# Optimization experiments

Hardware: AMD Instinct MI355X
Metric: run time of the kernel (lower is better)

Reference implementation:

```python
import jax, jax.numpy as jnp
import numpy as np

B, S, D = 32, 4096, 256

def setup_inputs() -> dict:
    key = jax.random.key(0)
    k1, k2, k3 = jax.random.split(key, 3)
    inputs = jax.random.normal(k1, (B, S, D), dtype=jnp.float32)
    W = jax.random.normal(k2, (D, D), dtype=jnp.float32) * 0.05  # 'random_normal' init
    b = jnp.zeros((D,), dtype=jnp.float32)
    V = jax.random.normal(k3, (D, 1), dtype=jnp.float32) * 0.05
    return {"inputs": inputs, "W": W, "b": b, "V": V}

def reference(inputs, W, b, V):
    # score: [B,S,D] = tanh(inputs @ W + b)
    score = jnp.tanh(jnp.einsum('bsd,de->bse', inputs, W) + b)
    # logits: [B,S,1]; softmax over seq axis (axis=1)
    logits = jnp.einsum('bsd,do->bso', score, V)
    attn = jax.nn.softmax(logits, axis=1)            # [B,S,1]
    # weighted sum pooling over seq -> [B,D]
    context = jnp.sum(attn * inputs, axis=1)
    return context
```

## Files before the change

kernel.cpp:

```cpp
#include <hip/hip_runtime.h>
#include <hip/hip_bf16.h>

#define DD 256
#define SS 4096

typedef __bf16 bf16x8 __attribute__((ext_vector_type(8)));
typedef float  f32x4  __attribute__((ext_vector_type(4)));

__device__ __forceinline__ float fast_tanh(float x) {
  float e = exp2f(x * 2.885390081777927f);
  return 1.0f - 2.0f / (e + 1.0f);
}

template<int CTRL>
__device__ __forceinline__ float dpp_mov(float v) {
  return __int_as_float(__builtin_amdgcn_update_dpp(0, __float_as_int(v), CTRL, 0xF, 0xF, true));
}
__device__ __forceinline__ float row16_sum(float v) {
  v += dpp_mov<0xB1>(v);
  v += dpp_mov<0x4E>(v);
  v += dpp_mov<0x124>(v);
  v += dpp_mov<0x128>(v);
  return v;
}
__device__ __forceinline__ float row16_max(float v) {
  v = fmaxf(v, dpp_mov<0xB1>(v));
  v = fmaxf(v, dpp_mov<0x4E>(v));
  v = fmaxf(v, dpp_mov<0x124>(v));
  v = fmaxf(v, dpp_mov<0x128>(v));
  return v;
}

__global__ __launch_bounds__(256) void prep_kernel(
    const float* __restrict__ W, __bf16* __restrict__ WF)
{
  const int c = blockIdx.x * 256 + threadIdx.x;
  const int lane_c = c & 63;
  const int ks  = (c >> 6) & 7;
  const int n0  = c >> 9;
  const int col = n0 * 16 + (lane_c & 15);
  const int k0  = ks * 32 + (lane_c >> 4) * 8;
  const float* wp = W + k0 * DD + col;
  bf16x8 fr;
  #pragma unroll
  for (int i = 0; i < 8; ++i) fr[i] = (__bf16)wp[i * DD];
  *reinterpret_cast<bf16x8*>(WF + (size_t)c * 8) = fr;
}

#define PACK(dst, f0, f1) { \
  bf16x8 _fr; \
  _fr[0] = (__bf16)(f0).x; _fr[1] = (__bf16)(f0).y; \
  _fr[2] = (__bf16)(f0).z; _fr[3] = (__bf16)(f0).w; \
  _fr[4] = (__bf16)(f1).x; _fr[5] = (__bf16)(f1).y; \
  _fr[6] = (__bf16)(f1).z; _fr[7] = (__bf16)(f1).w; \
  (dst) = _fr; }

#define TILE(aX, spX, n0q) { \
  const __bf16* _bp = WtF + ((size_t)((n0q) * 8 * 64 + lane)) * 8; \
  bf16x8 _bfr[8]; \
  _Pragma("unroll") \
  for (int _ks = 0; _ks < 8; ++_ks) \
    _bfr[_ks] = *reinterpret_cast<const bf16x8*>(_bp + (size_t)_ks * 512); \
  f32x4 _acc = {0.f, 0.f, 0.f, 0.f}; \
  _Pragma("unroll") \
  for (int _ks = 0; _ks < 8; ++_ks) \
    _acc = __builtin_amdgcn_mfma_f32_16x16x32_bf16(aX[_ks], _bfr[_ks], _acc, 0, 0, 0); \
  const int _col = (n0q) * 16 + lg; \
  const float _vc = Vs[_col], _bc = Bs[_col]; \
  _Pragma("unroll") \
  for (int _r = 0; _r < 4; ++_r) \
    spX[_r] += fast_tanh(_acc[_r] + _bc) * _vc; }

__global__ __launch_bounds__(1024, 1) __attribute__((amdgpu_waves_per_eu(4)))
void fused_kernel(
    const float* __restrict__ X, const __bf16* __restrict__ WF,
    const float* __restrict__ bias, const float* __restrict__ V,
    float* __restrict__ Pout, float* __restrict__ Mout, float* __restrict__ Sout)
{
  __shared__ __bf16 WtF[8192 * 8];
  __shared__ float  Pacc[16][DD];
  __shared__ float  Vs[DD];
  __shared__ float  Bs[DD];
  __shared__ float  wred[16];
  __shared__ float  sred[16];

  const int t = threadIdx.x;
  const int wave = t >> 6, lane = t & 63;
  const int g  = lane >> 4;
  const int lg = lane & 15;
  const size_t rowBase = (size_t)blockIdx.x * 512 + (size_t)wave * 32;

  float4 raw[16];
  const float* xr0 = X + (rowBase + lg) * DD;
  #pragma unroll
  for (int ks = 0; ks < 8; ++ks) {
    const float4* p = reinterpret_cast<const float4*>(xr0 + ks * 32 + g * 8);
    raw[2 * ks]     = p[0];
    raw[2 * ks + 1] = p[1];
  }

  {
    const uint4* src = reinterpret_cast<const uint4*>(WF);
    uint4* dst = reinterpret_cast<uint4*>(WtF);
    #pragma unroll
    for (int i = 0; i < 8; ++i) dst[t + i * 1024] = src[t + i * 1024];
  }
  if (t < DD) { Vs[t] = V[t]; Bs[t] = bias[t]; }
  __syncthreads();

  bf16x8 a0[8], a1[8];
  #pragma unroll
  for (int ks = 0; ks < 8; ++ks) PACK(a0[ks], raw[2 * ks], raw[2 * ks + 1]);
  const float* xr1 = X + (rowBase + 16 + lg) * DD;
  #pragma unroll
  for (int ks = 0; ks < 4; ++ks) {
    const float4* p = reinterpret_cast<const float4*>(xr1 + ks * 32 + g * 8);
    raw[2 * ks]     = p[0];
    raw[2 * ks + 1] = p[1];
  }

  float sp0[4] = {0.f,0.f,0.f,0.f};
  float sp1[4] = {0.f,0.f,0.f,0.f};

  #pragma unroll 1
  for (int n0 = 0; n0 < 8; ++n0) TILE(a0, sp0, n0);

  #pragma unroll
  for (int ks = 0; ks < 4; ++ks) PACK(a1[ks], raw[2 * ks], raw[2 * ks + 1]);
  #pragma unroll
  for (int ks = 4; ks < 8; ++ks) {
    const float4* p = reinterpret_cast<const float4*>(xr1 + ks * 32 + g * 8);
    raw[2 * (ks - 4)]     = p[0];
    raw[2 * (ks - 4) + 1] = p[1];
  }

  #pragma unroll 1
  for (int n0 = 8; n0 < 16; ++n0) TILE(a0, sp0, n0);

  #pragma unroll
  for (int ks = 4; ks < 8; ++ks) PACK(a1[ks], raw[2 * (ks - 4)], raw[2 * (ks - 4) + 1]);

  #pragma unroll 1
  for (int n0 = 0; n0 < 16; ++n0) TILE(a1, sp1, n0);

  #pragma unroll
  for (int r = 0; r < 4; ++r) { sp0[r] = row16_sum(sp0[r]); sp1[r] = row16_sum(sp1[r]); }

  const int src = ((lg >> 2) << 4) | lg;
  float l0 = 0.f, l1 = 0.f;
  #pragma unroll
  for (int r = 0; r < 4; ++r) {
    float v0 = __shfl(sp0[r], src, 64);
    float v1 = __shfl(sp1[r], src, 64);
    if ((lg & 3) == r) { l0 = v0; l1 = v1; }
  }

  float wm = row16_max(fmaxf(l0, l1));
  if (lane == 0) wred[wave] = wm;
  __syncthreads();
  float M = -1e30f;
  #pragma unroll
  for (int w = 0; w < 16; ++w) M = fmaxf(M, wred[w]);

  const float w0 = __expf(l0 - M);
  const float w1 = __expf(l1 - M);

  float se = row16_sum(w0 + w1);
  if (lane == 0) sred[wave] = se;

  #pragma unroll
  for (int ks = 0; ks < 8; ++ks) {
    float p8[8];
    #pragma unroll
    for (int i = 0; i < 8; ++i)
      p8[i] = w0 * (float)a0[ks][i] + w1 * (float)a1[ks][i];
    #pragma unroll
    for (int i = 0; i < 8; ++i) p8[i] = row16_sum(p8[i]);
    if (lg < 2) {
      float4 v = (lg == 0) ? make_float4(p8[0], p8[1], p8[2], p8[3])
                           : make_float4(p8[4], p8[5], p8[6], p8[7]);
      *reinterpret_cast<float4*>(&Pacc[wave][ks * 32 + g * 8 + lg * 4]) = v;
    }
  }
  __syncthreads();

  if (t < DD) {
    float s = 0.f;
    #pragma unroll
    for (int w = 0; w < 16; ++w) s += Pacc[w][t];
    Pout[(size_t)blockIdx.x * DD + t] = s;
  }
  if (t == 0) {
    float ss = 0.f;
    #pragma unroll
    for (int w = 0; w < 16; ++w) ss += sred[w];
    Sout[blockIdx.x] = ss;
    Mout[blockIdx.x] = M;
  }
}

__global__ __launch_bounds__(256) void combine_kernel(
    const float* __restrict__ P, const float* __restrict__ Mb,
    const float* __restrict__ Sb, float* __restrict__ ctx)
{
  const int b = blockIdx.x, t = threadIdx.x;
  float Mg = -1e30f;
  #pragma unroll
  for (int k = 0; k < 8; ++k) Mg = fmaxf(Mg, Mb[b * 8 + k]);
  float denom = 0.f, acc = 0.f;
  #pragma unroll
  for (int k = 0; k < 8; ++k) {
    const float f = __expf(Mb[b * 8 + k] - Mg);
    denom += f * Sb[b * 8 + k];
    acc   += f * P[(size_t)(b * 8 + k) * DD + t];
  }
  ctx[b * DD + t] = acc / denom;
}

extern "C" void kernel_launch(void* const* d_in, const int* in_sizes, int n_in,
                              void* d_out, int out_size, void* d_ws, size_t ws_size,
                              hipStream_t stream) {
  const float* X    = (const float*)d_in[0];
  const float* W    = (const float*)d_in[1];
  const float* bias = (const float*)d_in[2];
  const float* V    = (const float*)d_in[3];
  float* ctx = (float*)d_out;

  __bf16* WF = (__bf16*)d_ws;
  float* P = (float*)((char*)d_ws + 128 * 1024);
  float* M = P + 256 * DD;
  float* S = M + 256;

  prep_kernel<<<32, 256, 0, stream>>>(W, WF);
  fused_kernel<<<256, 1024, 0, stream>>>(X, WF, bias, V, P, M, S);
  combine_kernel<<<32, 256, 0, stream>>>(P, M, S, ctx);
}
```

Baseline: 60.04 us.

## Use online softmax per row-group to reuse a single A fragment buffer

Replaces the two live bf16 A-fragment arrays with one. Each 16-row group is folded into per-wave running max, sum and Pacc accumulators with online-softmax rescaling, and a per-block rescale merges the waves at the end. Scheduling barriers are added to pin where the global loads sit. The aim is to cut register pressure so that loads overlap better with compute, at the cost of extra exp and rescale work and read-modify-write traffic on shared memory.

Measured after the change: 66.16 us. 10.2% more time.

```diff
diff --git a/kernel.cpp b/kernel.cpp
--- a/kernel.cpp
+++ b/kernel.cpp
@@ -70,6 +70,40 @@
   _Pragma("unroll") \
   for (int _r = 0; _r < 4; ++_r) \
     spX[_r] += fast_tanh(_acc[_r] + _bc) * _vc; }
+
+#define PHASE3(aX, spX) { \
+  _Pragma("unroll") \
+  for (int _r = 0; _r < 4; ++_r) spX[_r] = row16_sum(spX[_r]); \
+  const int _src = ((lg >> 2) << 4) | lg; \
+  float _l0 = 0.f; \
+  _Pragma("unroll") \
+  for (int _r = 0; _r < 4; ++_r) { \
+    float _v0 = __shfl(spX[_r], _src, 64); \
+    if ((lg & 3) == _r) _l0 = _v0; \
+  } \
+  const float _mc = row16_max(_l0); \
+  const float _Mn = fmaxf(Mrun, _mc); \
+  const float _f  = __expf(Mrun - _Mn); \
+  Mrun = _Mn; \
+  const float _w0 = __expf(_l0 - _Mn); \
+  Srun = Srun * _f + row16_sum(_w0); \
+  _Pragma("unroll") \
+  for (int _ks = 0; _ks < 8; ++_ks) { \
+    float _p8[8]; \
+    _Pragma("unroll") \
+    for (int _i = 0; _i < 8; ++_i) _p8[_i] = _w0 * (float)aX[_ks][_i]; \
+    _Pragma("unroll") \
+    for (int _i = 0; _i < 8; ++_i) _p8[_i] = row16_sum(_p8[_i]); \
+    if (lg < 2) { \
+      float4 _nv = (lg == 0) ? make_float4(_p8[0], _p8[1], _p8[2], _p8[3]) \
+                             : make_float4(_p8[4], _p8[5], _p8[6], _p8[7]); \
+      float4* _pp = reinterpret_cast<float4*>(&Pacc[wave][_ks * 32 + g * 8 + lg * 4]); \
+      float4 _ov = *_pp; \
+      _ov.x = _f * _ov.x + _nv.x; _ov.y = _f * _ov.y + _nv.y; \
+      _ov.z = _f * _ov.z + _nv.z; _ov.w = _f * _ov.w + _nv.w; \
+      *_pp = _ov; \
+    } \
+  } }
 
 __global__ __launch_bounds__(1024, 1) __attribute__((amdgpu_waves_per_eu(4)))
 void fused_kernel(
@@ -98,6 +132,7 @@
     raw[2 * ks]     = p[0];
     raw[2 * ks + 1] = p[1];
   }
+  __builtin_amdgcn_sched_barrier(0);
 
   {
     const uint4* src = reinterpret_cast<const uint4*>(WF);
@@ -106,11 +141,19 @@
     for (int i = 0; i < 8; ++i) dst[t + i * 1024] = src[t + i * 1024];
   }
   if (t < DD) { Vs[t] = V[t]; Bs[t] = bias[t]; }
+  {
+    float* pz = &Pacc[0][0];
+    #pragma unroll
+    for (int i = 0; i < 4; ++i) pz[t + i * 1024] = 0.f;
+  }
   __syncthreads();
 
-  bf16x8 a0[8], a1[8];
-  #pragma unroll
-  for (int ks = 0; ks < 8; ++ks) PACK(a0[ks], raw[2 * ks], raw[2 * ks + 1]);
+  float Mrun = -1e30f, Srun = 0.f;
+
+  bf16x8 a[8];
+  #pragma unroll
+  for (int ks = 0; ks < 8; ++ks) PACK(a[ks], raw[2 * ks], raw[2 * ks + 1]);
+
   const float* xr1 = X + (rowBase + 16 + lg) * DD;
   #pragma unroll
   for (int ks = 0; ks < 4; ++ks) {
@@ -118,84 +161,52 @@
     raw[2 * ks]     = p[0];
     raw[2 * ks + 1] = p[1];
   }
-
-  float sp0[4] = {0.f,0.f,0.f,0.f};
-  float sp1[4] = {0.f,0.f,0.f,0.f};
-
+  __builtin_amdgcn_sched_barrier(0);
+
+  float sp[4] = {0.f, 0.f, 0.f, 0.f};
   #pragma unroll 1
-  for (int n0 = 0; n0 < 8; ++n0) TILE(a0, sp0, n0);
-
-  #pragma unroll
-  for (int ks = 0; ks < 4; ++ks) PACK(a1[ks], raw[2 * ks], raw[2 * ks + 1]);
+  for (int n0 = 0; n0 < 8; ++n0) TILE(a, sp, n0);
+
   #pragma unroll
   for (int ks = 4; ks < 8; ++ks) {
     const float4* p = reinterpret_cast<const float4*>(xr1 + ks * 32 + g * 8);
-    raw[2 * (ks - 4)]     = p[0];
-    raw[2 * (ks - 4) + 1] = p[1];
-  }
+    raw[2 * ks]     = p[0];
+    raw[2 * ks + 1] = p[1];
+  }
+  __builtin_amdgcn_sched_barrier(0);
 
   #pragma unroll 1
-  for (int n0 = 8; n0 < 16; ++n0) TILE(a0, sp0, n0);
-
-  #pragma unroll
-  for (int ks = 4; ks < 8; ++ks) PACK(a1[ks], raw[2 * (ks - 4)], raw[2 * (ks - 4) + 1]);
-
+  for (int n0 = 8; n0 < 16; ++n0) TILE(a, sp, n0);
+
+  PHASE3(a, sp);
+
+  #pragma unroll
+  for (int ks = 0; ks < 8; ++ks) PACK(a[ks], raw[2 * ks], raw[2 * ks + 1]);
+
+  float sq[4] = {0.f, 0.f, 0.f, 0.f};
   #pragma unroll 1
-  for (int n0 = 0; n0 < 16; ++n0) TILE(a1, sp1, n0);
-
-  #pragma unroll
-  for (int r = 0; r < 4; ++r) { sp0[r] = row16_sum(sp0[r]); sp1[r] = row16_sum(sp1[r]); }
-
-  const int src = ((lg >> 2) << 4) | lg;
-  float l0 = 0.f, l1 = 0.f;
-  #pragma unroll
-  for (int r = 0; r < 4; ++r) {
-    float v0 = __shfl(sp0[r], src, 64);
-    float v1 = __shfl(sp1[r], src, 64);
-    if ((lg & 3) == r) { l0 = v0; l1 = v1; }
-  }
-
-  float wm = row16_max(fmaxf(l0, l1));
-  if (lane == 0) wred[wave] = wm;
+  for (int n0 = 0; n0 < 16; ++n0) TILE(a, sq, n0);
+
+  PHASE3(a, sq);
+
+  if (lane == 0) { wred[wave] = Mrun; sred[wave] = Srun; }
   __syncthreads();
-  float M = -1e30f;
-  #pragma unroll
-  for (int w = 0; w < 16; ++w) M = fmaxf(M, wred[w]);
-
-  const float w0 = __expf(l0 - M);
-  const float w1 = __expf(l1 - M);
-
-  float se = row16_sum(w0 + w1);
-  if (lane == 0) sred[wave] = se;
-
-  #pragma unroll
-  for (int ks = 0; ks < 8; ++ks) {
-    float p8[8];
-    #pragma unroll
-    for (int i = 0; i < 8; ++i)
-      p8[i] = w0 * (float)a0[ks][i] + w1 * (float)a1[ks][i];
-    #pragma unroll
-    for (int i = 0; i < 8; ++i) p8[i] = row16_sum(p8[i]);
-    if (lg < 2) {
-      float4 v = (lg == 0) ? make_float4(p8[0], p8[1], p8[2], p8[3])
-                           : make_float4(p8[4], p8[5], p8[6], p8[7]);
-      *reinterpret_cast<float4*>(&Pacc[wave][ks * 32 + g * 8 + lg * 4]) = v;
-    }
-  }
-  __syncthreads();
-
+
+  float MB = -1e30f;
+  #pragma unroll
+  for (int w = 0; w < 16; ++w) MB = fmaxf(MB, wred[w]);
   if (t < DD) {
     float s = 0.f;
     #pragma unroll
-    for (int w = 0; w < 16; ++w) s += Pacc[w][t];
+    for (int w = 0; w < 16; ++w) s += __expf(wred[w] - MB) * Pacc[w][t];
     Pout[(size_t)blockIdx.x * DD + t] = s;
   }
   if (t == 0) {
     float ss = 0.f;
     #pragma unroll
-    for (int w = 0; w < 16; ++w) ss += sred[w];
+    for (int w = 0; w < 16; ++w) ss += __expf(wred[w] - MB) * sred[w];
     Sout[blockIdx.x] = ss;
-    Mout[blockIdx.x] = M;
+    Mout[blockIdx.x] = MB;
   }
 }
 
```
